# Kernel optimization log

Hardware: AMD Instinct MI355X
Metric: run time of the kernel (lower is better)

Reference implementation:

```python
import jax, jax.numpy as jnp
import numpy as np

DIM = 128        # per-head dim == model width in this module
Q_HEADS = 16
KV_HEADS = 4
WINDOW = 512
BATCH = 4
SEQ = 2048


def setup_inputs() -> dict:
    key = jax.random.key(0)
    k1, k2, k3 = jax.random.split(key, 3)
    x = jax.random.normal(k1, (BATCH, SEQ, DIM), dtype=jnp.float32)
    # fused qkv weight, stored (in, out) so forward is x @ W_qkv
    W_qkv = jax.random.normal(k2, (DIM, (Q_HEADS + 2 * KV_HEADS) * DIM), dtype=jnp.float32) * (DIM ** -0.5)
    W_proj = jax.random.normal(k3, (Q_HEADS * DIM, DIM), dtype=jnp.float32) * ((Q_HEADS * DIM) ** -0.5)
    return {"x": x, "W_qkv": W_qkv, "W_proj": W_proj}


def _gqa_forward(x, W_qkv, W_proj):
    b, s, d = x.shape
    qkv = x @ W_qkv                                    # [b, s, (Hq+2Hkv)*d]
    qkv = qkv.reshape(b, s, Q_HEADS + 2 * KV_HEADS, d).transpose(0, 2, 1, 3)
    q = qkv[:, :Q_HEADS]                               # [b, Hq, s, d]
    k = qkv[:, Q_HEADS:Q_HEADS + KV_HEADS]             # [b, Hkv, s, d]
    v = qkv[:, Q_HEADS + KV_HEADS:]                    # [b, Hkv, s, d]

    # GQA: repeat kv heads to match q heads
    group = Q_HEADS // KV_HEADS
    k = jnp.repeat(k, group, axis=1)                   # [b, Hq, s, d]
    v = jnp.repeat(v, group, axis=1)

    scale = 1.0 / jnp.sqrt(jnp.float32(d))
    scores = jnp.einsum('bhqd,bhkd->bhqk', q, k) * scale   # [b, Hq, s, s]

    q_idx = jnp.arange(s)[:, None]
    kv_idx = jnp.arange(s)[None, :]
    rel = (q_idx - kv_idx).astype(jnp.float32)         # [s, s]
    # per-head ALiBi slope: exp2(-(h+1)*8/Hq), added (sign matches source)
    h = jnp.arange(Q_HEADS, dtype=jnp.float32)
    slopes = jnp.exp2(-((h + 1.0) * 8.0 / Q_HEADS))    # [Hq]
    scores = scores + slopes[None, :, None, None] * rel[None, None, :, :]

    mask = (q_idx >= kv_idx) & ((q_idx - kv_idx) <= WINDOW)
    scores = jnp.where(mask[None, None], scores, -jnp.inf)
    probs = jax.nn.softmax(scores, axis=-1)

    att = jnp.einsum('bhqk,bhkd->bhqd', probs, v)      # [b, Hq, s, d]
    att = att.transpose(0, 2, 1, 3).reshape(b, s, Q_HEADS * d)
    return att @ W_proj                                # [b, s, d]


def reference(x, W_qkv, W_proj):
    return _gqa_forward(x, W_qkv, W_proj)
```

## Files before the change

### kernel.cpp

```cpp
#include <hip/hip_runtime.h>
#include <math.h>

#define DIM_    128
#define QH_     16
#define KVH_    4
#define WIN_    512
#define BATCH_  4
#define SEQ_    2048
#define QKV_LD  3072
#define ATT_LD  2048

#define NX   (BATCH_*SEQ_*DIM_)
#define NWQ  (DIM_*QKV_LD)
#define NWP  (ATT_LD*DIM_)

typedef __attribute__((ext_vector_type(8))) short short8;
typedef __attribute__((ext_vector_type(4))) float f32x4;
typedef unsigned short u16;
typedef unsigned int u32;

__device__ __forceinline__ u16 f2bf(float f) {
    u32 u = __float_as_uint(f);
    u += 0x7fff + ((u >> 16) & 1);
    return (u16)(u >> 16);
}
__device__ __forceinline__ float bf2f(u16 u) {
    return __uint_as_float(((u32)u) << 16);
}
#define MFMA16 __builtin_amdgcn_mfma_f32_16x16x32_bf16

#if __has_builtin(__builtin_amdgcn_exp2f)
#define EXP2F __builtin_amdgcn_exp2f
#else
#define EXP2F exp2f
#endif

__device__ __forceinline__ void gload_lds16(const u16* g, u16* l) {
    __builtin_amdgcn_global_load_lds(
        (const __attribute__((address_space(1))) unsigned int*)(const void*)g,
        (__attribute__((address_space(3))) unsigned int*)(void*)l, 16, 0, 0);
}

__global__ __launch_bounds__(256) void convert_inputs(
    const float* __restrict__ x, const float* __restrict__ Wqkv,
    const float* __restrict__ Wproj,
    u16* __restrict__ xh, u16* __restrict__ wth, u16* __restrict__ wpth)
{
    const int t = blockIdx.x * 256 + threadIdx.x;
    if (t < NX) {
        xh[t] = f2bf(x[t]);
    } else if (t < NX + NWQ) {
        const int u2 = t - NX;
        const int k = u2 & 127, n = u2 >> 7;
        wth[u2] = f2bf(Wqkv[(size_t)k * QKV_LD + n]);
    } else {
        const int u2 = t - NX - NWQ;
        const int k = u2 & 2047, n = u2 >> 11;
        wpth[u2] = f2bf(Wproj[(size_t)k * DIM_ + n]);
    }
}

__global__ __launch_bounds__(256) void gemm1_mfma(
    const u16* __restrict__ xh, const u16* __restrict__ wth,
    u16* __restrict__ qkvb, u16* __restrict__ vg)
{
    __shared__ u16 Ab[32][512];
    __shared__ u16 Bb[16][512];
    const int bn = blockIdx.x * 64;
    const int bm = blockIdx.y * 128;
    const int tid = threadIdx.x;
    const int wv = tid >> 6, lane = tid & 63;
    const int lr = lane & 15, quad = lane >> 4;
    const int lo = lane & 15, hi = lane >> 4;

    #pragma unroll
    for (int i = 0; i < 12; ++i) {
        const int idx = wv * 12 + i;
        if (idx < 32) {
            const int mt = idx >> 2, s = idx & 3;
            gload_lds16(xh + (size_t)(bm + mt * 16 + lo) * DIM_ + s * 32 + hi * 8,
                        &Ab[idx][0]);
        } else {
            const int j = idx - 32, nt = j >> 2, s = j & 3;
            gload_lds16(wth + (size_t)(bn + nt * 16 + lo) * DIM_ + s * 32 + hi * 8,
                        &Bb[j][0]);
        }
    }
    __syncthreads();

    const int wr = wv >> 1, wc = wv & 1;
    f32x4 acc[4][2] = {};
    if (bn < 2560) {
        #pragma unroll
        for (int s = 0; s < 4; ++s) {
            short8 af[4], bf[2];
            #pragma unroll
            for (int mt = 0; mt < 4; ++mt)
                af[mt] = *(const short8*)&Ab[(wr * 4 + mt) * 4 + s][lane * 8];
            #pragma unroll
            for (int nt = 0; nt < 2; ++nt)
                bf[nt] = *(const short8*)&Bb[(wc * 2 + nt) * 4 + s][lane * 8];
            #pragma unroll
            for (int mt = 0; mt < 4; ++mt)
                #pragma unroll
                for (int nt = 0; nt < 2; ++nt)
                    acc[mt][nt] = MFMA16(bf[nt], af[mt], acc[mt][nt], 0, 0, 0);
        }
        #pragma unroll
        for (int mt = 0; mt < 4; ++mt)
            #pragma unroll
            for (int nt = 0; nt < 2; ++nt) {
                ushort4 o;
                o.x = f2bf(acc[mt][nt][0]); o.y = f2bf(acc[mt][nt][1]);
                o.z = f2bf(acc[mt][nt][2]); o.w = f2bf(acc[mt][nt][3]);
                *(ushort4*)(qkvb
                    + (size_t)(bm + wr * 64 + mt * 16 + lr) * QKV_LD
                    + bn + wc * 32 + nt * 16 + quad * 4) = o;
            }
    } else {
        #pragma unroll
        for (int s = 0; s < 4; ++s) {
            short8 af[4], bf[2];
            #pragma unroll
            for (int mt = 0; mt < 4; ++mt)
                af[mt] = *(const short8*)&Ab[(wr * 4 + mt) * 4 + s][lane * 8];
            #pragma unroll
            for (int nt = 0; nt < 2; ++nt)
                bf[nt] = *(const short8*)&Bb[(wc * 2 + nt) * 4 + s][lane * 8];
            #pragma unroll
            for (int mt = 0; mt < 4; ++mt)
                #pragma unroll
                for (int nt = 0; nt < 2; ++nt)
                    acc[mt][nt] = MFMA16(af[mt], bf[nt], acc[mt][nt], 0, 0, 0);
        }
        #pragma unroll
        for (int mt = 0; mt < 4; ++mt)
            #pragma unroll
            for (int nt = 0; nt < 2; ++nt) {
                const int ncol = bn + wc * 32 + nt * 16 + lr - 2560;
                const int kvh = ncol >> 7, d = ncol & 127;
                const int m0 = bm + wr * 64 + mt * 16 + quad * 4;
                ushort4 o;
                o.x = f2bf(acc[mt][nt][0]); o.y = f2bf(acc[mt][nt][1]);
                o.z = f2bf(acc[mt][nt][2]); o.w = f2bf(acc[mt][nt][3]);
                *(ushort4*)(vg + ((size_t)((m0 >> 11) * KVH_ + kvh) * DIM_ + d)
                            * SEQ_ + (m0 & 2047)) = o;
            }
    }
}

__global__ __launch_bounds__(256) void attn_mfma(
    const u16* __restrict__ qkvb, const u16* __restrict__ vg,
    u16* __restrict__ ah)
{
    const int qt = blockIdx.x, kvh = blockIdx.y, b = blockIdx.z;
    const int q0 = qt << 5;
    const int tid = threadIdx.x;
    const int wv = tid >> 6, lane = tid & 63;
    const int lr = lane & 15, quad = lane >> 4;
    const int h = kvh * 4 + wv;

    __shared__ u16 Kb[4][8][512];
    __shared__ u16 Vb[4][8][512];
    __shared__ u16 Pt[4][32][36];

    const float scale2 = 0.08838834764831845f * 1.4426950408889634f;
    const float slope2 = exp2f(-0.5f * (float)(h + 1)) * 1.4426950408889634f;
    const int jbase = max(0, q0 - WIN_);
    const int nch = (q0 + 32 - jbase) >> 5;
    const size_t rowb = (size_t)b * SEQ_;
    const u16* kg  = qkvb + rowb * QKV_LD + (QH_ + kvh) * DIM_;
    const u16* vgb = vg + (size_t)(b * KVH_ + kvh) * DIM_ * SEQ_;
    const int lo = lane & 15, hi = lane >> 4;

    short8 qf[2][4];
    #pragma unroll
    for (int m = 0; m < 2; ++m) {
        const u16* qp = qkvb + (rowb + q0 + m * 16 + lr) * QKV_LD
                        + h * DIM_ + quad * 8;
        #pragma unroll
        for (int s = 0; s < 4; ++s) qf[m][s] = *(const short8*)(qp + 32 * s);
    }

    float alpha[2];
    #pragma unroll
    for (int m = 0; m < 2; ++m) {
        const int q = q0 + m * 16 + lr;
        const int rm = (q < WIN_) ? q : WIN_;
        alpha[m] = slope2 * (float)(q - rm);
    }

    f32x4 O[2][8] = {};
    float rs[2] = {0.f, 0.f};

    #define STAGE(CH, SLOT) do {                                              \
        const int _jk = jbase + ((CH) << 5);                                  \
        _Pragma("unroll")                                                     \
        for (int _t = 0; _t < 2; ++_t) {                                      \
            const int _p = wv + _t * 4;                                       \
            gload_lds16(kg + (size_t)(_jk + (_p >> 2) * 16 + lo) * QKV_LD     \
                        + (_p & 3) * 32 + hi * 8, &Kb[(SLOT)][_p][0]);        \
            gload_lds16(vgb + (size_t)(_p * 16 + lo) * SEQ_ + _jk + hi * 8,   \
                        &Vb[(SLOT)][_p][0]);                                  \
        }                                                                     \
    } while (0)

    STAGE(0, 0);
    { const int c1 = (1 < nch) ? 1 : (nch - 1); STAGE(c1, 1); }

    for (int ch = 0; ch < nch; ++ch) {
        const int jk = jbase + (ch << 5);
        const int slot = ch & 3;
        { const int cn = (ch + 2 < nch) ? (ch + 2) : (nch - 1);
          STAGE(cn, (ch + 2) & 3); }
        __asm__ volatile("s_waitcnt vmcnt(8)" ::: "memory");
        __asm__ volatile("s_barrier" ::: "memory");

        #pragma unroll
        for (int nt = 0; nt < 2; ++nt) {
            f32x4 c0 = {0.f, 0.f, 0.f, 0.f}, c1 = {0.f, 0.f, 0.f, 0.f};
            #pragma unroll
            for (int s = 0; s < 4; ++s) {
                short8 kf = *(const short8*)&Kb[slot][nt * 4 + s][lane * 8];
                c0 = MFMA16(kf, qf[0][s], c0, 0, 0, 0);
                c1 = MFMA16(kf, qf[1][s], c1, 0, 0, 0);
            }
            const int jknt = jk + nt * 16;
            #pragma unroll
            for (int m = 0; m < 2; ++m) {
                const f32x4 c = m ? c1 : c0;
                const int qm0 = q0 + m * 16;
                const float b0 = fmaf(-slope2, (float)(jknt + quad * 4), alpha[m]);
                float e0, e1, e2, e3;
                if (qm0 >= jknt + 15 && qm0 + 15 <= jknt + WIN_) {
                    e0 = EXP2F(fmaf(c[0], scale2, b0));
                    e1 = EXP2F(fmaf(c[1], scale2, b0 - slope2));
                    e2 = EXP2F(fmaf(c[2], scale2, b0 - 2.f * slope2));
                    e3 = EXP2F(fmaf(c[3], scale2, b0 - 3.f * slope2));
                } else {
                    const int q = qm0 + lr, j0q = jknt + quad * 4;
                    float ee[4];
                    #pragma unroll
                    for (int r = 0; r < 4; ++r) {
                        const int rel = q - (j0q + r);
                        const float t = fmaf(c[r], scale2, b0 - (float)r * slope2);
                        ee[r] = ((unsigned)rel <= (unsigned)WIN_) ? EXP2F(t) : 0.f;
                    }
                    e0 = ee[0]; e1 = ee[1]; e2 = ee[2]; e3 = ee[3];
                }
                rs[m] += (e0 + e1) + (e2 + e3);
                ushort4 o;
                o.x = f2bf(e0); o.y = f2bf(e1); o.z = f2bf(e2); o.w = f2bf(e3);
                *(ushort4*)&Pt[wv][m * 16 + lr][nt * 16 + quad * 4] = o;
            }
        }
        __asm__ volatile("s_waitcnt lgkmcnt(0)" ::: "memory");

        short8 pa0 = *(const short8*)&Pt[wv][lr][quad * 8];
        short8 pa1 = *(const short8*)&Pt[wv][16 + lr][quad * 8];
        #pragma unroll
        for (int nt = 0; nt < 8; ++nt) {
            short8 vf = *(const short8*)&Vb[slot][nt][lane * 8];
            O[0][nt] = MFMA16(vf, pa0, O[0][nt], 0, 0, 0);
            O[1][nt] = MFMA16(vf, pa1, O[1][nt], 0, 0, 0);
        }
    }
    #undef STAGE

    __asm__ volatile("s_waitcnt vmcnt(0)" ::: "memory");

    #pragma unroll
    for (int m = 0; m < 2; ++m) {
        rs[m] += __shfl_xor(rs[m], 16);
        rs[m] += __shfl_xor(rs[m], 32);
    }

    #pragma unroll
    for (int m = 0; m < 2; ++m) {
        const float inv = 1.0f / rs[m];
        u16* dst = ah + (rowb + q0 + m * 16 + lr) * (size_t)ATT_LD + h * DIM_;
        #pragma unroll
        for (int nt = 0; nt < 8; ++nt) {
            ushort4 o;
            o.x = f2bf(O[m][nt][0] * inv); o.y = f2bf(O[m][nt][1] * inv);
            o.z = f2bf(O[m][nt][2] * inv); o.w = f2bf(O[m][nt][3] * inv);
            *(ushort4*)(dst + nt * 16 + quad * 4) = o;
        }
    }
}

__global__ __launch_bounds__(512) void gemm2_mfma(
    const u16* __restrict__ ah, const u16* __restrict__ wpth,
    float* __restrict__ out)
{
    const int bm = blockIdx.x * 32;
    const int tid = threadIdx.x;
    const int wv = tid >> 6, lane = tid & 63;
    const int lr = lane & 15, quad = lane >> 4;
    const int mt = wv & 1, cq = wv >> 1;

    const u16* arow  = ah + (size_t)(bm + mt * 16 + lr) * ATT_LD + quad * 8;
    const u16* w0row = wpth + (size_t)(cq * 32 + lr) * ATT_LD + quad * 8;
    const u16* w1row = w0row + (size_t)16 * ATT_LD;

    f32x4 acc0 = {0.f, 0.f, 0.f, 0.f}, acc1 = {0.f, 0.f, 0.f, 0.f};
    #pragma unroll 4
    for (int k0 = 0; k0 < ATT_LD; k0 += 32) {
        short8 a  = *(const short8*)(arow + k0);
        short8 w0 = *(const short8*)(w0row + k0);
        short8 w1 = *(const short8*)(w1row + k0);
        acc0 = MFMA16(w0, a, acc0, 0, 0, 0);
        acc1 = MFMA16(w1, a, acc1, 0, 0, 0);
    }
    float* orow = out + (size_t)(bm + mt * 16 + lr) * DIM_ + cq * 32;
    *(float4*)(orow + quad * 4)      = *(float4*)&acc0;
    *(float4*)(orow + 16 + quad * 4) = *(float4*)&acc1;
}

extern "C" void kernel_launch(void* const* d_in, const int* in_sizes, int n_in,
                              void* d_out, int out_size, void* d_ws, size_t ws_size,
                              hipStream_t stream)
{
    const float* x     = (const float*)d_in[0];
    const float* Wqkv  = (const float*)d_in[1];
    const float* Wproj = (const float*)d_in[2];
    float* out = (float*)d_out;

    u16* xh   = (u16*)d_ws;
    u16* wth  = xh   + (size_t)NX;
    u16* wpth = wth  + (size_t)NWQ;
    u16* qkvb = wpth + (size_t)NWP;
    u16* vg   = qkvb + (size_t)8192 * QKV_LD;
    u16* ahp  = vg   + (size_t)BATCH_ * KVH_ * DIM_ * SEQ_;

    convert_inputs<<<(NX + NWQ + NWP) / 256, 256, 0, stream>>>(
        x, Wqkv, Wproj, xh, wth, wpth);

    gemm1_mfma<<<dim3(QKV_LD / 64, 8192 / 128), 256, 0, stream>>>(
        xh, wth, qkvb, vg);

    attn_mfma<<<dim3(SEQ_ / 32, KVH_, BATCH_), 256, 0, stream>>>(qkvb, vg, ahp);

    gemm2_mfma<<<8192 / 32, 512, 0, stream>>>(ahp, wpth, out);
}
```

Baseline: 209.3 us.

## Split attention loop into 16-key K steps with interleaved V loads and triple buffering

The attention main loop now steps over 16-key chunks instead of 32. K tiles are loaded each step and V tiles every other step, with dummy loads into a trash LDS buffer keeping the vmcnt accounting uniform. The P·V MFMA runs only on odd steps, after two score tiles have filled the P buffer. Buffers shrink from 4-deep to 3-deep to cut LDS use, which may raise occupancy, at the cost of more barriers per key and extra dummy global loads.

```diff
diff --git a/kernel.cpp b/kernel.cpp
--- a/kernel.cpp
+++ b/kernel.cpp
@@ -160,14 +160,16 @@
     const int lr = lane & 15, quad = lane >> 4;
     const int h = kvh * 4 + wv;
 
-    __shared__ u16 Kb[4][8][512];
-    __shared__ u16 Vb[4][8][512];
+    __shared__ u16 Kb[3][4][512];
+    __shared__ u16 Vb[3][8][512];
     __shared__ u16 Pt[4][32][36];
+    __shared__ u16 Trash[512];
 
     const float scale2 = 0.08838834764831845f * 1.4426950408889634f;
     const float slope2 = exp2f(-0.5f * (float)(h + 1)) * 1.4426950408889634f;
     const int jbase = max(0, q0 - WIN_);
-    const int nch = (q0 + 32 - jbase) >> 5;
+    const int nch = (q0 + 32 - jbase) >> 4;
+    const int nv  = nch >> 1;
     const size_t rowb = (size_t)b * SEQ_;
     const u16* kg  = qkvb + rowb * QKV_LD + (QH_ + kvh) * DIM_;
     const u16* vgb = vg + (size_t)(b * KVH_ + kvh) * DIM_ * SEQ_;
@@ -193,79 +195,90 @@
     f32x4 O[2][8] = {};
     float rs[2] = {0.f, 0.f};
 
-    #define STAGE(CH, SLOT) do {                                              \
-        const int _jk = jbase + ((CH) << 5);                                  \
+    #define STAGE_K(C) gload_lds16(                                           \
+        kg + (size_t)(jbase + ((C) << 4) + lo) * QKV_LD + wv * 32 + hi * 8,   \
+        &Kb[(C) % 3][wv][0])
+    #define STAGE_V(VC) do {                                                  \
+        const int _jv = jbase + ((VC) << 5);                                  \
         _Pragma("unroll")                                                     \
         for (int _t = 0; _t < 2; ++_t) {                                      \
             const int _p = wv + _t * 4;                                       \
-            gload_lds16(kg + (size_t)(_jk + (_p >> 2) * 16 + lo) * QKV_LD     \
-                        + (_p & 3) * 32 + hi * 8, &Kb[(SLOT)][_p][0]);        \
-            gload_lds16(vgb + (size_t)(_p * 16 + lo) * SEQ_ + _jk + hi * 8,   \
-                        &Vb[(SLOT)][_p][0]);                                  \
+            gload_lds16(vgb + (size_t)(_p * 16 + lo) * SEQ_ + _jv + hi * 8,   \
+                        &Vb[(VC) % 3][_p][0]);                                \
         }                                                                     \
     } while (0)
-
-    STAGE(0, 0);
-    { const int c1 = (1 < nch) ? 1 : (nch - 1); STAGE(c1, 1); }
+    #define STAGE_T() do {                                                    \
+        gload_lds16(vgb + (size_t)lo * SEQ_ + hi * 8, &Trash[0]);             \
+        gload_lds16(vgb + (size_t)lo * SEQ_ + hi * 8, &Trash[0]);             \
+    } while (0)
+
+    STAGE_K(0);
+    STAGE_V(0);
 
     for (int ch = 0; ch < nch; ++ch) {
-        const int jk = jbase + (ch << 5);
-        const int slot = ch & 3;
-        { const int cn = (ch + 2 < nch) ? (ch + 2) : (nch - 1);
-          STAGE(cn, (ch + 2) & 3); }
-        __asm__ volatile("s_waitcnt vmcnt(8)" ::: "memory");
+        { const int kc = (ch + 1 < nch) ? ch + 1 : nch - 1; STAGE_K(kc); }
+        if (!(ch & 1)) {
+            const int vc = ((ch >> 1) + 1 < nv) ? (ch >> 1) + 1 : nv - 1;
+            STAGE_V(vc);
+        } else {
+            STAGE_T();
+        }
+        __asm__ volatile("s_waitcnt vmcnt(5)" ::: "memory");
         __asm__ volatile("s_barrier" ::: "memory");
 
-        #pragma unroll
-        for (int nt = 0; nt < 2; ++nt) {
-            f32x4 c0 = {0.f, 0.f, 0.f, 0.f}, c1 = {0.f, 0.f, 0.f, 0.f};
-            #pragma unroll
-            for (int s = 0; s < 4; ++s) {
-                short8 kf = *(const short8*)&Kb[slot][nt * 4 + s][lane * 8];
-                c0 = MFMA16(kf, qf[0][s], c0, 0, 0, 0);
-                c1 = MFMA16(kf, qf[1][s], c1, 0, 0, 0);
+        const int ks = ch % 3;
+        f32x4 c0 = {0.f, 0.f, 0.f, 0.f}, c1 = {0.f, 0.f, 0.f, 0.f};
+        #pragma unroll
+        for (int s = 0; s < 4; ++s) {
+            short8 kf = *(const short8*)&Kb[ks][s][lane * 8];
+            c0 = MFMA16(kf, qf[0][s], c0, 0, 0, 0);
+            c1 = MFMA16(kf, qf[1][s], c1, 0, 0, 0);
+        }
+        const int jk = jbase + (ch << 4);
+        #pragma unroll
+        for (int m = 0; m < 2; ++m) {
+            const f32x4 c = m ? c1 : c0;
+            const int qm0 = q0 + m * 16;
+            const float b0 = fmaf(-slope2, (float)(jk + quad * 4), alpha[m]);
+            float e0, e1, e2, e3;
+            if (qm0 >= jk + 15 && qm0 + 15 <= jk + WIN_) {
+                e0 = EXP2F(fmaf(c[0], scale2, b0));
+                e1 = EXP2F(fmaf(c[1], scale2, b0 - slope2));
+                e2 = EXP2F(fmaf(c[2], scale2, b0 - 2.f * slope2));
+                e3 = EXP2F(fmaf(c[3], scale2, b0 - 3.f * slope2));
+            } else {
+                const int q = qm0 + lr, j0q = jk + quad * 4;
+                float ee[4];
+                #pragma unroll
+                for (int r = 0; r < 4; ++r) {
+                    const int rel = q - (j0q + r);
+                    const float t = fmaf(c[r], scale2, b0 - (float)r * slope2);
+                    ee[r] = ((unsigned)rel <= (unsigned)WIN_) ? EXP2F(t) : 0.f;
+                }
+                e0 = ee[0]; e1 = ee[1]; e2 = ee[2]; e3 = ee[3];
             }
-            const int jknt = jk + nt * 16;
-            #pragma unroll
-            for (int m = 0; m < 2; ++m) {
-                const f32x4 c = m ? c1 : c0;
-                const int qm0 = q0 + m * 16;
-                const float b0 = fmaf(-slope2, (float)(jknt + quad * 4), alpha[m]);
-                float e0, e1, e2, e3;
-                if (qm0 >= jknt + 15 && qm0 + 15 <= jknt + WIN_) {
-                    e0 = EXP2F(fmaf(c[0], scale2, b0));
-                    e1 = EXP2F(fmaf(c[1], scale2, b0 - slope2));
-                    e2 = EXP2F(fmaf(c[2], scale2, b0 - 2.f * slope2));
-                    e3 = EXP2F(fmaf(c[3], scale2, b0 - 3.f * slope2));
-                } else {
-                    const int q = qm0 + lr, j0q = jknt + quad * 4;
-                    float ee[4];
-                    #pragma unroll
-                    for (int r = 0; r < 4; ++r) {
-                        const int rel = q - (j0q + r);
-                        const float t = fmaf(c[r], scale2, b0 - (float)r * slope2);
-                        ee[r] = ((unsigned)rel <= (unsigned)WIN_) ? EXP2F(t) : 0.f;
-                    }
-                    e0 = ee[0]; e1 = ee[1]; e2 = ee[2]; e3 = ee[3];
-                }
-                rs[m] += (e0 + e1) + (e2 + e3);
-                ushort4 o;
-                o.x = f2bf(e0); o.y = f2bf(e1); o.z = f2bf(e2); o.w = f2bf(e3);
-                *(ushort4*)&Pt[wv][m * 16 + lr][nt * 16 + quad * 4] = o;
+            rs[m] += (e0 + e1) + (e2 + e3);
+            ushort4 o;
+            o.x = f2bf(e0); o.y = f2bf(e1); o.z = f2bf(e2); o.w = f2bf(e3);
+            *(ushort4*)&Pt[wv][m * 16 + lr][(ch & 1) * 16 + quad * 4] = o;
+        }
+
+        if (ch & 1) {
+            __asm__ volatile("s_waitcnt lgkmcnt(0)" ::: "memory");
+            const int vs = (ch >> 1) % 3;
+            short8 pa0 = *(const short8*)&Pt[wv][lr][quad * 8];
+            short8 pa1 = *(const short8*)&Pt[wv][16 + lr][quad * 8];
+            #pragma unroll
+            for (int nt = 0; nt < 8; ++nt) {
+                short8 vf = *(const short8*)&Vb[vs][nt][lane * 8];
+                O[0][nt] = MFMA16(vf, pa0, O[0][nt], 0, 0, 0);
+                O[1][nt] = MFMA16(vf, pa1, O[1][nt], 0, 0, 0);
             }
         }
-        __asm__ volatile("s_waitcnt lgkmcnt(0)" ::: "memory");
-
-        short8 pa0 = *(const short8*)&Pt[wv][lr][quad * 8];
-        short8 pa1 = *(const short8*)&Pt[wv][16 + lr][quad * 8];
-        #pragma unroll
-        for (int nt = 0; nt < 8; ++nt) {
-            short8 vf = *(const short8*)&Vb[slot][nt][lane * 8];
-            O[0][nt] = MFMA16(vf, pa0, O[0][nt], 0, 0, 0);
-            O[1][nt] = MFMA16(vf, pa1, O[1][nt], 0, 0, 0);
-        }
-    }
-    #undef STAGE
+    }
+    #undef STAGE_K
+    #undef STAGE_V
+    #undef STAGE_T
 
     __asm__ volatile("s_waitcnt vmcnt(0)" ::: "memory");
 
```

Measured after the change: 234.4 us. +12.0%, slower.

## Split input conversion into vectorized cast and tiled weight transpose; shrink gemm2 blocks

Applied to the files above, without the earlier changes.

Replaces the single scalar conversion kernel, whose weight transposes read with strided uncoalesced loads, with two kernels. One casts x to bf16 using float4 loads and ushort4 stores. The other transposes and casts both weight matrices through 32x32 LDS tiles so reads and writes are coalesced. gemm2 now uses 16-row, 256-thread blocks with deeper unrolling, giving twice as many blocks at the cost of more redundant weight reads and one extra kernel launch.

```diff
diff --git a/kernel.cpp b/kernel.cpp
--- a/kernel.cpp
+++ b/kernel.cpp
@@ -41,23 +41,35 @@
         (__attribute__((address_space(3))) unsigned int*)(void*)l, 16, 0, 0);
 }
 
-__global__ __launch_bounds__(256) void convert_inputs(
-    const float* __restrict__ x, const float* __restrict__ Wqkv,
-    const float* __restrict__ Wproj,
-    u16* __restrict__ xh, u16* __restrict__ wth, u16* __restrict__ wpth)
-{
-    const int t = blockIdx.x * 256 + threadIdx.x;
-    if (t < NX) {
-        xh[t] = f2bf(x[t]);
-    } else if (t < NX + NWQ) {
-        const int u2 = t - NX;
-        const int k = u2 & 127, n = u2 >> 7;
-        wth[u2] = f2bf(Wqkv[(size_t)k * QKV_LD + n]);
-    } else {
-        const int u2 = t - NX - NWQ;
-        const int k = u2 & 2047, n = u2 >> 11;
-        wpth[u2] = f2bf(Wproj[(size_t)k * DIM_ + n]);
-    }
+__global__ __launch_bounds__(256) void xcvt(
+    const float* __restrict__ x, u16* __restrict__ xh)
+{
+    const size_t t = (size_t)blockIdx.x * 256 + threadIdx.x;
+    float4 v = *(const float4*)(x + 4 * t);
+    ushort4 o;
+    o.x = f2bf(v.x); o.y = f2bf(v.y); o.z = f2bf(v.z); o.w = f2bf(v.w);
+    *(ushort4*)(xh + 4 * t) = o;
+}
+
+__global__ __launch_bounds__(256) void wtrans(
+    const float* __restrict__ Wqkv, const float* __restrict__ Wproj,
+    u16* __restrict__ wth, u16* __restrict__ wpth)
+{
+    __shared__ float T[32][33];
+    int tile = blockIdx.x;
+    const float* src; u16* dst; int K, N;
+    if (tile < 384) { src = Wqkv;  dst = wth;  K = 128;  N = 3072; }
+    else { tile -= 384; src = Wproj; dst = wpth; K = 2048; N = 128; }
+    const int ntile = N >> 5;
+    const int k0 = (tile / ntile) << 5, n0 = (tile % ntile) << 5;
+    const int tx = threadIdx.x & 31, ty = threadIdx.x >> 5;
+    #pragma unroll
+    for (int i = 0; i < 4; ++i)
+        T[ty + 8 * i][tx] = src[(size_t)(k0 + ty + 8 * i) * N + n0 + tx];
+    __syncthreads();
+    #pragma unroll
+    for (int i = 0; i < 4; ++i)
+        dst[(size_t)(n0 + ty + 8 * i) * K + k0 + tx] = f2bf(T[tx][ty + 8 * i]);
 }
 
 __global__ __launch_bounds__(256) void gemm1_mfma(
@@ -289,22 +301,21 @@
     }
 }
 
-__global__ __launch_bounds__(512) void gemm2_mfma(
+__global__ __launch_bounds__(256) void gemm2_mfma(
     const u16* __restrict__ ah, const u16* __restrict__ wpth,
     float* __restrict__ out)
 {
-    const int bm = blockIdx.x * 32;
-    const int tid = threadIdx.x;
-    const int wv = tid >> 6, lane = tid & 63;
+    const int bm = blockIdx.x * 16;
+    const int wv = threadIdx.x >> 6, lane = threadIdx.x & 63;
     const int lr = lane & 15, quad = lane >> 4;
-    const int mt = wv & 1, cq = wv >> 1;
-
-    const u16* arow  = ah + (size_t)(bm + mt * 16 + lr) * ATT_LD + quad * 8;
+    const int cq = wv;
+
+    const u16* arow  = ah + (size_t)(bm + lr) * ATT_LD + quad * 8;
     const u16* w0row = wpth + (size_t)(cq * 32 + lr) * ATT_LD + quad * 8;
     const u16* w1row = w0row + (size_t)16 * ATT_LD;
 
     f32x4 acc0 = {0.f, 0.f, 0.f, 0.f}, acc1 = {0.f, 0.f, 0.f, 0.f};
-    #pragma unroll 4
+    #pragma unroll 8
     for (int k0 = 0; k0 < ATT_LD; k0 += 32) {
         short8 a  = *(const short8*)(arow + k0);
         short8 w0 = *(const short8*)(w0row + k0);
@@ -312,7 +323,7 @@
         acc0 = MFMA16(w0, a, acc0, 0, 0, 0);
         acc1 = MFMA16(w1, a, acc1, 0, 0, 0);
     }
-    float* orow = out + (size_t)(bm + mt * 16 + lr) * DIM_ + cq * 32;
+    float* orow = out + (size_t)(bm + lr) * DIM_ + cq * 32;
     *(float4*)(orow + quad * 4)      = *(float4*)&acc0;
     *(float4*)(orow + 16 + quad * 4) = *(float4*)&acc1;
 }
@@ -333,13 +344,13 @@
     u16* vg   = qkvb + (size_t)8192 * QKV_LD;
     u16* ahp  = vg   + (size_t)BATCH_ * KVH_ * DIM_ * SEQ_;
 
-    convert_inputs<<<(NX + NWQ + NWP) / 256, 256, 0, stream>>>(
-        x, Wqkv, Wproj, xh, wth, wpth);
+    xcvt<<<NX / 1024, 256, 0, stream>>>(x, xh);
+    wtrans<<<384 + 256, 256, 0, stream>>>(Wqkv, Wproj, wth, wpth);
 
     gemm1_mfma<<<dim3(QKV_LD / 64, 8192 / 128), 256, 0, stream>>>(
         xh, wth, qkvb, vg);
 
     attn_mfma<<<dim3(SEQ_ / 32, KVH_, BATCH_), 256, 0, stream>>>(qkvb, vg, ahp);
 
-    gemm2_mfma<<<8192 / 32, 512, 0, stream>>>(ahp, wpth, out);
-}
+    gemm2_mfma<<<8192 / 16, 256, 0, stream>>>(ahp, wpth, out);
+}
```

New measurement: 207.9 us. About the same (-0.7%).
